# Optimization experiments

Hardware: AMD Instinct MI355X
Metric: run time of the kernel (lower is better)

## Reference

```python
import jax, jax.numpy as jnp
import numpy as np

EPS = 1e-5

def setup_inputs() -> dict:
    key = jax.random.key(0)
    ks = jax.random.split(key, 5)
    B, T, D = 2, 4096, 512
    x = jax.random.normal(ks[0], (B, T, D), dtype=jnp.float32)
    w_qkv = jax.random.normal(ks[1], (D, 3 * D), dtype=jnp.float32) * (1.0 / np.sqrt(D))
    w_out = jax.random.normal(ks[2], (D, D), dtype=jnp.float32) * (1.0 / np.sqrt(D))
    b_out = jnp.zeros((D,), dtype=jnp.float32)
    gamma = jnp.ones((D,), dtype=jnp.float32)
    beta = jnp.zeros((D,), dtype=jnp.float32)
    return {"x": x, "w_qkv": w_qkv, "w_out": w_out, "b_out": b_out,
            "gamma": gamma, "beta": beta}

def reference(x, w_qkv, w_out, b_out, gamma, beta):
    B, T, D = x.shape
    H = 8
    hd = D // H
    scale = 1.0 / jnp.sqrt(jnp.asarray(hd, x.dtype))
    residual = x
    # pre-norm LayerNorm
    mu = jnp.mean(x, axis=-1, keepdims=True)
    var = jnp.mean((x - mu) ** 2, axis=-1, keepdims=True)
    xn = (x - mu) / jnp.sqrt(var + EPS) * gamma + beta
    # qkv projection (no bias)
    qkv = (xn @ w_qkv).reshape(B, T, 3, H, hd)
    q, k, v = qkv[:, :, 0], qkv[:, :, 1], qkv[:, :, 2]  # (B,T,H,hd)
    # (B,H,T,T) scores with causal mask
    attn = jnp.einsum('bthd,bshd->bhts', q, k) * scale
    causal = jnp.triu(jnp.ones((T, T), dtype=bool), k=1)
    attn = jnp.where(causal[None, None], -jnp.inf, attn)
    attn = jax.nn.softmax(attn, axis=-1)
    out = jnp.einsum('bhts,bshd->bthd', attn, v).reshape(B, T, D)
    out = out @ w_out + b_out
    return out + residual
```

## Files before the change

kernel.cpp:

```cpp
#include <hip/hip_runtime.h>

typedef __attribute__((ext_vector_type(8))) short bh8;
typedef __attribute__((ext_vector_type(4))) float f32x4;
typedef unsigned short u16;

#define MFMA16 __builtin_amdgcn_mfma_f32_16x16x32_bf16

#if __has_builtin(__builtin_amdgcn_exp2f)
#define EXP2(x) __builtin_amdgcn_exp2f(x)
#else
#define EXP2(x) exp2f(x)
#endif

#define CEXP 0.18033688011112042f

__device__ __forceinline__ u16 f2bf(float f) {
  union { float f; unsigned u; } v; v.f = f;
  unsigned r = v.u + 0x7fffu + ((v.u >> 16) & 1u);
  return (u16)(r >> 16);
}

__device__ __forceinline__ unsigned cvtpk(float lo, float hi) {
  unsigned r;
  asm("v_cvt_pk_bf16_f32 %0, %1, %2" : "=v"(r) : "v"(lo), "v"(hi));
  return r;
}

__device__ __forceinline__ void gload16(void* lds, const void* g) {
  __builtin_amdgcn_global_load_lds(
      (const __attribute__((address_space(1))) unsigned int*)g,
      (__attribute__((address_space(3))) unsigned int*)lds, 16, 0, 0);
}

__global__ __launch_bounds__(256) void k_ln(const float* __restrict__ x,
                                            const float* __restrict__ gamma,
                                            const float* __restrict__ beta,
                                            u16* __restrict__ xn) {
  int row  = blockIdx.x * 4 + (threadIdx.x >> 6);
  int lane = threadIdx.x & 63;
  const float4* xr = (const float4*)(x + row * 512);
  float4 a = xr[lane * 2], b = xr[lane * 2 + 1];
  float s  = a.x + a.y + a.z + a.w + b.x + b.y + b.z + b.w;
  float ss = a.x*a.x + a.y*a.y + a.z*a.z + a.w*a.w
           + b.x*b.x + b.y*b.y + b.z*b.z + b.w*b.w;
#pragma unroll
  for (int m = 1; m < 64; m <<= 1) { s += __shfl_xor(s, m, 64); ss += __shfl_xor(ss, m, 64); }
  float mu  = s * (1.0f / 512.0f);
  float var = ss * (1.0f / 512.0f) - mu * mu;
  float rstd = rsqrtf(var + 1e-5f);
  const float4* g4 = (const float4*)gamma;
  const float4* b4 = (const float4*)beta;
  float4 g0 = g4[lane * 2], g1 = g4[lane * 2 + 1];
  float4 e0 = b4[lane * 2], e1 = b4[lane * 2 + 1];
  bh8 ov;
  ov[0] = (short)f2bf((a.x - mu) * rstd * g0.x + e0.x);
  ov[1] = (short)f2bf((a.y - mu) * rstd * g0.y + e0.y);
  ov[2] = (short)f2bf((a.z - mu) * rstd * g0.z + e0.z);
  ov[3] = (short)f2bf((a.w - mu) * rstd * g0.w + e0.w);
  ov[4] = (short)f2bf((b.x - mu) * rstd * g1.x + e1.x);
  ov[5] = (short)f2bf((b.y - mu) * rstd * g1.y + e1.y);
  ov[6] = (short)f2bf((b.z - mu) * rstd * g1.z + e1.z);
  ov[7] = (short)f2bf((b.w - mu) * rstd * g1.w + e1.w);
  *(bh8*)(xn + row * 512 + lane * 8) = ov;
}

__global__ __launch_bounds__(256) void k_transpose_cast(const float* __restrict__ in,
                                                        u16* __restrict__ out,
                                                        int R, int C) {
  __shared__ float tile[32][33];
  int c0 = blockIdx.x * 32, r0 = blockIdx.y * 32;
  int tx = threadIdx.x & 31, ty = threadIdx.x >> 5;
#pragma unroll
  for (int i = 0; i < 32; i += 8)
    tile[ty + i][tx] = in[(r0 + ty + i) * C + (c0 + tx)];
  __syncthreads();
#pragma unroll
  for (int i = 0; i < 32; i += 8)
    out[(c0 + ty + i) * R + (r0 + tx)] = f2bf(tile[tx][ty + i]);
}

template <int EPI>
__global__ __launch_bounds__(256) void k_gemm(const u16* __restrict__ A,
                                              const u16* __restrict__ Bt,
                                              int N,
                                              u16* __restrict__ q, u16* __restrict__ kk, u16* __restrict__ vt,
                                              const float* __restrict__ bias,
                                              const float* __restrict__ resid,
                                              float* __restrict__ outp) {
  constexpr int K = 512, BM = 128, BK = 64;
  __shared__ u16 Al[BM * BK];
  __shared__ u16 Bl[BM * BK];
  int nBN = N / 128;
  int bid = (blockIdx.x & 7) * (gridDim.x >> 3) + (blockIdx.x >> 3);
  int m0 = (bid / nBN) * BM;
  int n0 = (bid % nBN) * 128;
  int tid = threadIdx.x, lane = tid & 63, w = tid >> 6;
  int l16 = lane & 15, lh = lane >> 4;
  int wm = (w >> 1) * 64, wn = (w & 1) * 64;
  const u16* Ab = A + m0 * K;
  const u16* Bb = Bt + n0 * K;
  f32x4 acc[4][4];
#pragma unroll
  for (int i = 0; i < 4; ++i)
#pragma unroll
    for (int j = 0; j < 4; ++j) acc[i][j] = (f32x4){0.f, 0.f, 0.f, 0.f};
  int srow = tid >> 3, schunk = tid & 7;
  for (int k0 = 0; k0 < K; k0 += BK) {
    __syncthreads();
#pragma unroll
    for (int j = 0; j < 4; ++j) {
      int r = j * 32 + srow;
      int sc = ((schunk ^ (r & 7)) << 3);
      gload16((char*)Al + j * 4096 + tid * 16, Ab + r * K + k0 + sc);
      gload16((char*)Bl + j * 4096 + tid * 16, Bb + r * K + k0 + sc);
    }
    __syncthreads();
#pragma unroll
    for (int c = 0; c < 2; ++c) {
      bh8 af[4], bf[4];
#pragma unroll
      for (int i = 0; i < 4; ++i) {
        int ra = wm + i * 16 + l16;
        af[i] = *(const bh8*)&Al[ra * 64 + ((c * 32 + lh * 8) ^ ((ra & 7) << 3))];
        int rb = wn + i * 16 + l16;
        bf[i] = *(const bh8*)&Bl[rb * 64 + ((c * 32 + lh * 8) ^ ((rb & 7) << 3))];
      }
#pragma unroll
      for (int mi = 0; mi < 4; ++mi)
#pragma unroll
        for (int ni = 0; ni < 4; ++ni)
          acc[mi][ni] = MFMA16(af[mi], bf[ni], acc[mi][ni], 0, 0, 0);
    }
  }
  if (EPI == 0) {
#pragma unroll
    for (int mi = 0; mi < 4; ++mi)
#pragma unroll
      for (int ni = 0; ni < 4; ++ni) {
        int col = n0 + wn + ni * 16 + l16;
        int s = col >> 9, h = (col >> 6) & 7, d = col & 63;
        int row0 = m0 + wm + mi * 16 + lh * 4;
        int b = row0 >> 12, t0 = row0 & 4095;
        if (s == 2) {
          uint2 pk;
          pk.x = cvtpk(acc[mi][ni][0], acc[mi][ni][1]);
          pk.y = cvtpk(acc[mi][ni][2], acc[mi][ni][3]);
          *(uint2*)&vt[((size_t)((b << 3) + h) * 64 + d) * 4096 + t0] = pk;
        } else {
          u16* base = (s == 0 ? q : kk);
#pragma unroll
          for (int j = 0; j < 4; ++j)
            base[(((size_t)(b << 3) + h) * 4096 + t0 + j) * 64 + d] = f2bf(acc[mi][ni][j]);
        }
      }
  } else {
#pragma unroll
    for (int mi = 0; mi < 4; ++mi)
#pragma unroll
      for (int ni = 0; ni < 4; ++ni) {
        int col = n0 + wn + ni * 16 + l16;
        float bo = bias[col];
#pragma unroll
        for (int j = 0; j < 4; ++j) {
          int row = m0 + wm + mi * 16 + lh * 4 + j;
          outp[row * 512 + col] = acc[mi][ni][j] + bo + resid[row * 512 + col];
        }
      }
  }
}

__global__ __launch_bounds__(256) void k_attn(const u16* __restrict__ Q,
                                              const u16* __restrict__ Kg,
                                              const u16* __restrict__ Vt,
                                              u16* __restrict__ O) {
  __shared__ u16 Kl[2 * 64 * 64];
  __shared__ u16 Vl[2 * 64 * 64];
  __shared__ u16 Pl[4 * 1024];
  int bh = blockIdx.x & 15;
  int qi = 63 - (blockIdx.x >> 4);
  int tid = threadIdx.x, lane = tid & 63, w = tid >> 6;
  int l16 = lane & 15, lh = lane >> 4;
  const u16* Qb = Q + bh * 4096 * 64;
  const u16* Kb = Kg + bh * 4096 * 64;
  const u16* Vb = Vt + (size_t)bh * 64 * 4096;
  int q0 = qi * 64;
  int myq = q0 + w * 16 + l16;
  bh8 qf0 = *(const bh8*)(Qb + myq * 64 + lh * 8);
  bh8 qf1 = *(const bh8*)(Qb + myq * 64 + 32 + lh * 8);
  float m_ = -3e38f, l_ = 0.f;
  f32x4 acc[4];
#pragma unroll
  for (int dn = 0; dn < 4; ++dn) acc[dn] = (f32x4){0.f, 0.f, 0.f, 0.f};
  int srow = tid >> 3, schunk = tid & 7;
  u16* pw = Pl + w * 1024 + l16 * 64;
  int pswz = (l16 & 7) << 3;

  for (int kt = 0; kt <= qi; kt += 2) {
    __syncthreads();
#pragma unroll
    for (int t = 0; t < 2; ++t) {
      int kk = (kt + t) * 64;
#pragma unroll
      for (int j = 0; j < 2; ++j) {
        int r = j * 32 + srow;
        int sc = ((schunk ^ (r & 7)) << 3);
        gload16((char*)Kl + t * 8192 + j * 4096 + tid * 16, Kb + (kk + r) * 64 + sc);
        gload16((char*)Vl + t * 8192 + j * 4096 + tid * 16, Vb + r * 4096 + kk + sc);
      }
    }
    __syncthreads();
    int k0 = kt * 64;
    f32x4 s[8];
    __builtin_amdgcn_s_setprio(1);
#pragma unroll
    for (int g = 0; g < 8; ++g) {
      const u16* Kc = Kl + (g >> 2) * 4096;
      int r = (g & 3) * 16 + l16;
      bh8 kf0 = *(const bh8*)&Kc[r * 64 + ((lh * 8) ^ ((r & 7) << 3))];
      bh8 kf1 = *(const bh8*)&Kc[r * 64 + ((32 + lh * 8) ^ ((r & 7) << 3))];
      f32x4 z = (f32x4){0.f, 0.f, 0.f, 0.f};
      z = MFMA16(kf0, qf0, z, 0, 0, 0);
      z = MFMA16(kf1, qf1, z, 0, 0, 0);
      s[g] = z;
    }
    __builtin_amdgcn_s_setprio(0);
    if (kt + 2 > qi) {
#pragma unroll
      for (int g = 0; g < 8; ++g)
#pragma unroll
        for (int j = 0; j < 4; ++j) {
          int tk = k0 + g * 16 + lh * 4 + j;
          if (tk > myq) s[g][j] = -3e38f;
        }
    }
    float mg[8];
#pragma unroll
    for (int g = 0; g < 8; ++g)
      mg[g] = fmaxf(fmaxf(s[g][0], s[g][1]), fmaxf(s[g][2], s[g][3]));
    float mx = fmaxf(fmaxf(fmaxf(mg[0], mg[1]), fmaxf(mg[2], mg[3])),
                     fmaxf(fmaxf(mg[4], mg[5]), fmaxf(mg[6], mg[7])));
    mx = fmaxf(mx, __shfl_xor(mx, 16, 64));
    mx = fmaxf(mx, __shfl_xor(mx, 32, 64));
    float nm = fmaxf(m_, mx);
    float nmC = nm * CEXP;
    float rs = 0.f;
#pragma unroll
    for (int g = 0; g < 8; ++g) {
      float p0 = EXP2(fmaf(s[g][0], CEXP, -nmC));
      float p1 = EXP2(fmaf(s[g][1], CEXP, -nmC));
      float p2 = EXP2(fmaf(s[g][2], CEXP, -nmC));
      float p3 = EXP2(fmaf(s[g][3], CEXP, -nmC));
      rs += (p0 + p1) + (p2 + p3);
      s[g][0] = p0; s[g][1] = p1; s[g][2] = p2; s[g][3] = p3;
    }
    rs += __shfl_xor(rs, 16, 64);
    rs += __shfl_xor(rs, 32, 64);
    if (__any(mx > m_)) {
      float fac = EXP2(fmaf(m_, CEXP, -nmC));
      l_ = l_ * fac + rs;
      float f0 = __shfl(fac, lh * 4 + 0, 64);
      float f1 = __shfl(fac, lh * 4 + 1, 64);
      float f2 = __shfl(fac, lh * 4 + 2, 64);
      float f3 = __shfl(fac, lh * 4 + 3, 64);
#pragma unroll
      for (int dn = 0; dn < 4; ++dn) {
        acc[dn][0] *= f0; acc[dn][1] *= f1;
        acc[dn][2] *= f2; acc[dn][3] *= f3;
      }
    } else {
      l_ += rs;
    }
    m_ = nm;
#pragma unroll
    for (int h = 0; h < 2; ++h) {
#pragma unroll
      for (int f = 0; f < 4; ++f) {
        int g = h * 4 + f;
        uint2 pk;
        pk.x = cvtpk(s[g][0], s[g][1]);
        pk.y = cvtpk(s[g][2], s[g][3]);
        *(uint2*)&pw[(f * 16 + lh * 4) ^ pswz] = pk;
      }
      bh8 pa0 = *(const bh8*)&pw[(lh * 8) ^ pswz];
      bh8 pa1 = *(const bh8*)&pw[(32 + lh * 8) ^ pswz];
      const u16* Vc = Vl + h * 4096;
      __builtin_amdgcn_s_setprio(1);
#pragma unroll
      for (int dn = 0; dn < 4; ++dn) {
        int r = dn * 16 + l16;
        const u16* vr = Vc + r * 64;
        bh8 vb0 = *(const bh8*)&vr[(lh * 8) ^ ((r & 7) << 3)];
        bh8 vb1 = *(const bh8*)&vr[(32 + lh * 8) ^ ((r & 7) << 3)];
        acc[dn] = MFMA16(pa0, vb0, acc[dn], 0, 0, 0);
        acc[dn] = MFMA16(pa1, vb1, acc[dn], 0, 0, 0);
      }
      __builtin_amdgcn_s_setprio(0);
    }
  }
  float inv = 1.0f / l_;
  float i0 = __shfl(inv, lh * 4 + 0, 64);
  float i1 = __shfl(inv, lh * 4 + 1, 64);
  float i2 = __shfl(inv, lh * 4 + 2, 64);
  float i3 = __shfl(inv, lh * 4 + 3, 64);
  int b = bh >> 3, h = bh & 7;
#pragma unroll
  for (int j = 0; j < 4; ++j) {
    float iv = (j == 0 ? i0 : j == 1 ? i1 : j == 2 ? i2 : i3);
    int t = q0 + w * 16 + lh * 4 + j;
#pragma unroll
    for (int dn = 0; dn < 4; ++dn)
      O[(b * 4096 + t) * 512 + h * 64 + dn * 16 + l16] = f2bf(acc[dn][j] * iv);
  }
}

extern "C" void kernel_launch(void* const* d_in, const int* in_sizes, int n_in,
                              void* d_out, int out_size, void* d_ws, size_t ws_size,
                              hipStream_t stream) {
  const float* x     = (const float*)d_in[0];
  const float* w_qkv = (const float*)d_in[1];
  const float* w_out = (const float*)d_in[2];
  const float* b_out = (const float*)d_in[3];
  const float* gamma = (const float*)d_in[4];
  const float* beta  = (const float*)d_in[5];
  float* out = (float*)d_out;
  char* ws = (char*)d_ws;
  u16* xn    = (u16*)(ws);
  u16* wqkvT = (u16*)(ws + 8388608);
  u16* woutT = (u16*)(ws + 9961472);
  u16* q     = (u16*)(ws + 10485760);
  u16* k     = (u16*)(ws + 18874368);
  u16* vt    = (u16*)(ws + 27262976);
  u16* attn_out = xn;

  k_ln<<<2048, 256, 0, stream>>>(x, gamma, beta, xn);
  k_transpose_cast<<<dim3(48, 16), 256, 0, stream>>>(w_qkv, wqkvT, 512, 1536);
  k_transpose_cast<<<dim3(16, 16), 256, 0, stream>>>(w_out, woutT, 512, 512);
  k_gemm<0><<<64 * 12, 256, 0, stream>>>(xn, wqkvT, 1536, q, k, vt, nullptr, nullptr, nullptr);
  k_attn<<<1024, 256, 0, stream>>>(q, k, vt, attn_out);
  k_gemm<1><<<64 * 4, 256, 0, stream>>>(attn_out, woutT, 512, nullptr, nullptr, nullptr, b_out, x, out);
}
```

Baseline: 123.9 us.

## Pair mirrored causal query tiles per block to share K/V loads

Each attention block now handles two query tiles, i and 63-i, so every block does the same amount of causal work. The K/V tiles staged in shared memory are reused for both queries while the short tile is still active. This halves the grid and doubles the P scratch buffer and accumulator registers. The aim is to cut redundant K/V global loads and the tail imbalance from uneven causal lengths, at the cost of higher register pressure and fewer blocks in flight.

```diff
diff --git a/kernel.cpp b/kernel.cpp
--- a/kernel.cpp
+++ b/kernel.cpp
@@ -175,64 +175,35 @@
                                               u16* __restrict__ O) {
   __shared__ u16 Kl[2 * 64 * 64];
   __shared__ u16 Vl[2 * 64 * 64];
-  __shared__ u16 Pl[4 * 1024];
+  __shared__ u16 Pl[8 * 1024];
   int bh = blockIdx.x & 15;
-  int qi = 63 - (blockIdx.x >> 4);
+  int i  = blockIdx.x >> 4;
+  int qa = 63 - i, qb = i;
   int tid = threadIdx.x, lane = tid & 63, w = tid >> 6;
   int l16 = lane & 15, lh = lane >> 4;
   const u16* Qb = Q + bh * 4096 * 64;
   const u16* Kb = Kg + bh * 4096 * 64;
   const u16* Vb = Vt + (size_t)bh * 64 * 4096;
-  int q0 = qi * 64;
-  int myq = q0 + w * 16 + l16;
-  bh8 qf0 = *(const bh8*)(Qb + myq * 64 + lh * 8);
-  bh8 qf1 = *(const bh8*)(Qb + myq * 64 + 32 + lh * 8);
-  float m_ = -3e38f, l_ = 0.f;
-  f32x4 acc[4];
-#pragma unroll
-  for (int dn = 0; dn < 4; ++dn) acc[dn] = (f32x4){0.f, 0.f, 0.f, 0.f};
+  int q0a = qa * 64, q0b = qb * 64;
+  int myqA = q0a + w * 16 + l16;
+  int myqB = q0b + w * 16 + l16;
+  bh8 qA0 = *(const bh8*)(Qb + myqA * 64 + lh * 8);
+  bh8 qA1 = *(const bh8*)(Qb + myqA * 64 + 32 + lh * 8);
+  bh8 qB0 = *(const bh8*)(Qb + myqB * 64 + lh * 8);
+  bh8 qB1 = *(const bh8*)(Qb + myqB * 64 + 32 + lh * 8);
+  float mA = -3e38f, lA = 0.f, mB = -3e38f, lB = 0.f;
+  f32x4 accA[4], accB[4];
+#pragma unroll
+  for (int dn = 0; dn < 4; ++dn) {
+    accA[dn] = (f32x4){0.f, 0.f, 0.f, 0.f};
+    accB[dn] = (f32x4){0.f, 0.f, 0.f, 0.f};
+  }
   int srow = tid >> 3, schunk = tid & 7;
-  u16* pw = Pl + w * 1024 + l16 * 64;
+  u16* pwA = Pl + w * 2048 + l16 * 64;
+  u16* pwB = pwA + 1024;
   int pswz = (l16 & 7) << 3;
 
-  for (int kt = 0; kt <= qi; kt += 2) {
-    __syncthreads();
-#pragma unroll
-    for (int t = 0; t < 2; ++t) {
-      int kk = (kt + t) * 64;
-#pragma unroll
-      for (int j = 0; j < 2; ++j) {
-        int r = j * 32 + srow;
-        int sc = ((schunk ^ (r & 7)) << 3);
-        gload16((char*)Kl + t * 8192 + j * 4096 + tid * 16, Kb + (kk + r) * 64 + sc);
-        gload16((char*)Vl + t * 8192 + j * 4096 + tid * 16, Vb + r * 4096 + kk + sc);
-      }
-    }
-    __syncthreads();
-    int k0 = kt * 64;
-    f32x4 s[8];
-    __builtin_amdgcn_s_setprio(1);
-#pragma unroll
-    for (int g = 0; g < 8; ++g) {
-      const u16* Kc = Kl + (g >> 2) * 4096;
-      int r = (g & 3) * 16 + l16;
-      bh8 kf0 = *(const bh8*)&Kc[r * 64 + ((lh * 8) ^ ((r & 7) << 3))];
-      bh8 kf1 = *(const bh8*)&Kc[r * 64 + ((32 + lh * 8) ^ ((r & 7) << 3))];
-      f32x4 z = (f32x4){0.f, 0.f, 0.f, 0.f};
-      z = MFMA16(kf0, qf0, z, 0, 0, 0);
-      z = MFMA16(kf1, qf1, z, 0, 0, 0);
-      s[g] = z;
-    }
-    __builtin_amdgcn_s_setprio(0);
-    if (kt + 2 > qi) {
-#pragma unroll
-      for (int g = 0; g < 8; ++g)
-#pragma unroll
-        for (int j = 0; j < 4; ++j) {
-          int tk = k0 + g * 16 + lh * 4 + j;
-          if (tk > myq) s[g][j] = -3e38f;
-        }
-    }
+  auto softmax = [&](f32x4 (&s)[8], float& m_, float& l_, f32x4 (&ac)[4]) {
     float mg[8];
 #pragma unroll
     for (int g = 0; g < 8; ++g)
@@ -264,25 +235,94 @@
       float f3 = __shfl(fac, lh * 4 + 3, 64);
 #pragma unroll
       for (int dn = 0; dn < 4; ++dn) {
-        acc[dn][0] *= f0; acc[dn][1] *= f1;
-        acc[dn][2] *= f2; acc[dn][3] *= f3;
+        ac[dn][0] *= f0; ac[dn][1] *= f1;
+        ac[dn][2] *= f2; ac[dn][3] *= f3;
       }
     } else {
       l_ += rs;
     }
     m_ = nm;
+  };
+
+  for (int kt = 0; kt <= qa; kt += 2) {
+    __syncthreads();
+#pragma unroll
+    for (int t = 0; t < 2; ++t) {
+      int kk = (kt + t) * 64;
+#pragma unroll
+      for (int j = 0; j < 2; ++j) {
+        int r = j * 32 + srow;
+        int sc = ((schunk ^ (r & 7)) << 3);
+        gload16((char*)Kl + t * 8192 + j * 4096 + tid * 16, Kb + (kk + r) * 64 + sc);
+        gload16((char*)Vl + t * 8192 + j * 4096 + tid * 16, Vb + r * 4096 + kk + sc);
+      }
+    }
+    __syncthreads();
+    int k0 = kt * 64;
+    bool dual = (kt <= qb);
+    f32x4 sA[8], sB[8];
+    __builtin_amdgcn_s_setprio(1);
+#pragma unroll
+    for (int g = 0; g < 8; ++g) {
+      const u16* Kc = Kl + (g >> 2) * 4096;
+      int r = (g & 3) * 16 + l16;
+      bh8 kf0 = *(const bh8*)&Kc[r * 64 + ((lh * 8) ^ ((r & 7) << 3))];
+      bh8 kf1 = *(const bh8*)&Kc[r * 64 + ((32 + lh * 8) ^ ((r & 7) << 3))];
+      f32x4 z = (f32x4){0.f, 0.f, 0.f, 0.f};
+      z = MFMA16(kf0, qA0, z, 0, 0, 0);
+      z = MFMA16(kf1, qA1, z, 0, 0, 0);
+      sA[g] = z;
+      if (dual) {
+        f32x4 y = (f32x4){0.f, 0.f, 0.f, 0.f};
+        y = MFMA16(kf0, qB0, y, 0, 0, 0);
+        y = MFMA16(kf1, qB1, y, 0, 0, 0);
+        sB[g] = y;
+      }
+    }
+    __builtin_amdgcn_s_setprio(0);
+    if (kt + 2 > qa) {
+#pragma unroll
+      for (int g = 0; g < 8; ++g)
+#pragma unroll
+        for (int j = 0; j < 4; ++j) {
+          int tk = k0 + g * 16 + lh * 4 + j;
+          if (tk > myqA) sA[g][j] = -3e38f;
+        }
+    }
+    if (dual && kt + 2 > qb) {
+#pragma unroll
+      for (int g = 0; g < 8; ++g)
+#pragma unroll
+        for (int j = 0; j < 4; ++j) {
+          int tk = k0 + g * 16 + lh * 4 + j;
+          if (tk > myqB) sB[g][j] = -3e38f;
+        }
+    }
+    softmax(sA, mA, lA, accA);
+    if (dual) softmax(sB, mB, lB, accB);
 #pragma unroll
     for (int h = 0; h < 2; ++h) {
 #pragma unroll
       for (int f = 0; f < 4; ++f) {
         int g = h * 4 + f;
         uint2 pk;
-        pk.x = cvtpk(s[g][0], s[g][1]);
-        pk.y = cvtpk(s[g][2], s[g][3]);
-        *(uint2*)&pw[(f * 16 + lh * 4) ^ pswz] = pk;
-      }
-      bh8 pa0 = *(const bh8*)&pw[(lh * 8) ^ pswz];
-      bh8 pa1 = *(const bh8*)&pw[(32 + lh * 8) ^ pswz];
+        pk.x = cvtpk(sA[g][0], sA[g][1]);
+        pk.y = cvtpk(sA[g][2], sA[g][3]);
+        *(uint2*)&pwA[(f * 16 + lh * 4) ^ pswz] = pk;
+        if (dual) {
+          uint2 pb;
+          pb.x = cvtpk(sB[g][0], sB[g][1]);
+          pb.y = cvtpk(sB[g][2], sB[g][3]);
+          *(uint2*)&pwB[(f * 16 + lh * 4) ^ pswz] = pb;
+        }
+      }
+      bh8 paA0 = *(const bh8*)&pwA[(lh * 8) ^ pswz];
+      bh8 paA1 = *(const bh8*)&pwA[(32 + lh * 8) ^ pswz];
+      bh8 paB0, paB1;
+      if (dual) {
+        paB0 = *(const bh8*)&pwB[(lh * 8) ^ pswz];
+        paB1 = *(const bh8*)&pwB[(32 + lh * 8) ^ pswz];
+      }
       const u16* Vc = Vl + h * 4096;
       __builtin_amdgcn_s_setprio(1);
 #pragma unroll
@@ -291,25 +331,46 @@
         const u16* vr = Vc + r * 64;
         bh8 vb0 = *(const bh8*)&vr[(lh * 8) ^ ((r & 7) << 3)];
         bh8 vb1 = *(const bh8*)&vr[(32 + lh * 8) ^ ((r & 7) << 3)];
-        acc[dn] = MFMA16(pa0, vb0, acc[dn], 0, 0, 0);
-        acc[dn] = MFMA16(pa1, vb1, acc[dn], 0, 0, 0);
+        accA[dn] = MFMA16(paA0, vb0, accA[dn], 0, 0, 0);
+        accA[dn] = MFMA16(paA1, vb1, accA[dn], 0, 0, 0);
+        if (dual) {
+          accB[dn] = MFMA16(paB0, vb0, accB[dn], 0, 0, 0);
+          accB[dn] = MFMA16(paB1, vb1, accB[dn], 0, 0, 0);
+        }
       }
       __builtin_amdgcn_s_setprio(0);
     }
   }
-  float inv = 1.0f / l_;
-  float i0 = __shfl(inv, lh * 4 + 0, 64);
-  float i1 = __shfl(inv, lh * 4 + 1, 64);
-  float i2 = __shfl(inv, lh * 4 + 2, 64);
-  float i3 = __shfl(inv, lh * 4 + 3, 64);
   int b = bh >> 3, h = bh & 7;
-#pragma unroll
-  for (int j = 0; j < 4; ++j) {
-    float iv = (j == 0 ? i0 : j == 1 ? i1 : j == 2 ? i2 : i3);
-    int t = q0 + w * 16 + lh * 4 + j;
-#pragma unroll
-    for (int dn = 0; dn < 4; ++dn)
-      O[(b * 4096 + t) * 512 + h * 64 + dn * 16 + l16] = f2bf(acc[dn][j] * iv);
+  {
+    float inv = 1.0f / lA;
+    float i0 = __shfl(inv, lh * 4 + 0, 64);
+    float i1 = __shfl(inv, lh * 4 + 1, 64);
+    float i2 = __shfl(inv, lh * 4 + 2, 64);
+    float i3 = __shfl(inv, lh * 4 + 3, 64);
+#pragma unroll
+    for (int j = 0; j < 4; ++j) {
+      float iv = (j == 0 ? i0 : j == 1 ? i1 : j == 2 ? i2 : i3);
+      int t = q0a + w * 16 + lh * 4 + j;
+#pragma unroll
+      for (int dn = 0; dn < 4; ++dn)
+        O[(b * 4096 + t) * 512 + h * 64 + dn * 16 + l16] = f2bf(accA[dn][j] * iv);
+    }
+  }
+  {
+    float inv = 1.0f / lB;
+    float i0 = __shfl(inv, lh * 4 + 0, 64);
+    float i1 = __shfl(inv, lh * 4 + 1, 64);
+    float i2 = __shfl(inv, lh * 4 + 2, 64);
+    float i3 = __shfl(inv, lh * 4 + 3, 64);
+#pragma unroll
+    for (int j = 0; j < 4; ++j) {
+      float iv = (j == 0 ? i0 : j == 1 ? i1 : j == 2 ? i2 : i3);
+      int t = q0b + w * 16 + lh * 4 + j;
+#pragma unroll
+      for (int dn = 0; dn < 4; ++dn)
+        O[(b * 4096 + t) * 512 + h * 64 + dn * 16 + l16] = f2bf(accB[dn][j] * iv);
+    }
   }
 }
 
@@ -336,6 +397,6 @@
   k_transpose_cast<<<dim3(48, 16), 256, 0, stream>>>(w_qkv, wqkvT, 512, 1536);
   k_transpose_cast<<<dim3(16, 16), 256, 0, stream>>>(w_out, woutT, 512, 512);
   k_gemm<0><<<64 * 12, 256, 0, stream>>>(xn, wqkvT, 1536, q, k, vt, nullptr, nullptr, nullptr);
-  k_attn<<<1024, 256, 0, stream>>>(q, k, vt, attn_out);
+  k_attn<<<512, 256, 0, stream>>>(q, k, vt, attn_out);
   k_gemm<1><<<64 * 4, 256, 0, stream>>>(attn_out, woutT, 512, nullptr, nullptr, nullptr, b_out, x, out);
 }
```

New measurement: 196.0 us. +58.2%, slower.
